# Performance work log

Hardware: AMD Instinct MI355X
Metric: run time of the kernel (lower is better)

The kernel has to match this reference:

```python
import jax, jax.numpy as jnp
import numpy as np

N = 100000      # nodes
E = 1600000     # directed edges (avg degree 16)
DIN, DH, DOUT = 128, 128, 64


def gcn_conv(x, W, b, src, dst, n):
    """PyG GCNConv: out = D^{-1/2} (A + I) D^{-1/2} (x @ W) + b.
    src/dst already include self-loops."""
    deg = jax.ops.segment_sum(jnp.ones_like(src, dtype=x.dtype), dst, num_segments=n)
    dinv = jnp.where(deg > 0, jax.lax.rsqrt(deg), jnp.zeros_like(deg))
    norm = dinv[src] * dinv[dst]                      # [E+N]
    h = x @ W                                         # [N, dout] linear first (PyG)
    msg = h[src] * norm[:, None]                      # gather + scale, [E+N, dout]
    return jax.ops.segment_sum(msg, dst, num_segments=n) + b


def setup_inputs() -> dict:
    key = jax.random.key(0)
    k1, k2, k3 = jax.random.split(key, 3)
    x = jax.random.normal(k1, (N, DIN), dtype=jnp.float32)
    edge_index = jax.random.randint(k2, (2, E), 0, N, dtype=jnp.int64)
    kw1, kw2 = jax.random.split(k3)
    # glorot-style init for the two GCN linear weights
    W1 = jax.random.normal(kw1, (DIN, DH), dtype=jnp.float32) * (1.0 / np.sqrt(DIN))
    b1 = jnp.zeros((DH,), dtype=jnp.float32)
    W2 = jax.random.normal(kw2, (DH, DOUT), dtype=jnp.float32) * (1.0 / np.sqrt(DH))
    b2 = jnp.zeros((DOUT,), dtype=jnp.float32)
    return {"x": x, "W1": W1, "b1": b1, "W2": W2, "b2": b2, "edge_index": edge_index}


def reference(x, W1, b1, W2, b2, edge_index):
    n = x.shape[0]
    loops = jnp.arange(n, dtype=edge_index.dtype)
    src = jnp.concatenate([edge_index[0], loops])     # add self-loops
    dst = jnp.concatenate([edge_index[1], loops])
    h = jax.nn.relu(gcn_conv(x, W1, b1, src, dst, n))
    return gcn_conv(h, W2, b2, src, dst, n)
```

## Files before the change

kernel.cpp:

```cpp
#include <hip/hip_runtime.h>

#define N_NODES 100000
#define N_EDGES 1600000
#define BUCKET_SHIFT 7
#define NB 782
#define BIN_BLOCKS 782
#define GEMM_BLOCKS 1563
#define BCAP 2816
#define AGG1_BLOCKS 3125
#define AGG2_BLOCKS 3125

typedef short bf16x8 __attribute__((ext_vector_type(8)));
typedef float f32x4 __attribute__((ext_vector_type(4)));
typedef float f32x8 __attribute__((ext_vector_type(8)));

__device__ __forceinline__ unsigned short f2bf(float f) {
    unsigned int u = __float_as_uint(f);
    unsigned int r = (u + 0x7FFFu + ((u >> 16) & 1u)) >> 16;
    return (unsigned short)r;
}
__device__ __forceinline__ float bf2f(unsigned short b) {
    return __uint_as_float(((unsigned int)b) << 16);
}
__device__ __forceinline__ void acc8(float* a, uint4 v) {
    a[0] += __uint_as_float(v.x << 16);
    a[1] += __uint_as_float(v.x & 0xFFFF0000u);
    a[2] += __uint_as_float(v.y << 16);
    a[3] += __uint_as_float(v.y & 0xFFFF0000u);
    a[4] += __uint_as_float(v.z << 16);
    a[5] += __uint_as_float(v.z & 0xFFFF0000u);
    a[6] += __uint_as_float(v.w << 16);
    a[7] += __uint_as_float(v.w & 0xFFFF0000u);
}

__global__ __launch_bounds__(256) void k_tw(const float* __restrict__ W1, const float* __restrict__ W2,
                                            unsigned short* __restrict__ w1t, unsigned short* __restrict__ w2t,
                                            int* __restrict__ bcur, int* __restrict__ gcount) {
    int t = blockIdx.x * 256 + threadIdx.x;
    if (t < 16384) {
        int k = t >> 7, c = t & 127;
        w1t[c * 128 + k] = f2bf(W1[t]);
    } else if (t < 24576) {
        int i = t - 16384;
        int k = i >> 6, c = i & 63;
        w2t[c * 128 + k] = f2bf(W2[i]);
    } else if (t - 24576 < NB) {
        bcur[t - 24576] = 0;
    } else if (t - 24576 == NB) {
        *gcount = 0;
    }
}

__global__ __launch_bounds__(256) void k_bin(const int* __restrict__ src, const int* __restrict__ dst,
                                             int* __restrict__ bcur, int* __restrict__ ebuf) {
    __shared__ int hist[NB];
    __shared__ int lbase[NB];
    int t = threadIdx.x;
    int e0 = blockIdx.x * 2048 + t;
    int s[8], d[8];
#pragma unroll
    for (int j = 0; j < 8; ++j) {
        int e = e0 + j * 256;
        bool ok = e < N_EDGES;
        s[j] = ok ? src[e] : -1;
        d[j] = ok ? dst[e] : 0;
    }
    for (int i = t; i < NB; i += 256) hist[i] = 0;
    __syncthreads();
#pragma unroll
    for (int j = 0; j < 8; ++j)
        if (s[j] >= 0) atomicAdd(&hist[d[j] >> BUCKET_SHIFT], 1);
    __syncthreads();
    for (int i = t; i < NB; i += 256)
        if (hist[i] > 0) lbase[i] = atomicAdd(&bcur[i], hist[i]);
    __syncthreads();
    for (int i = t; i < NB; i += 256) hist[i] = 0;
    __syncthreads();
#pragma unroll
    for (int j = 0; j < 8; ++j) {
        if (s[j] >= 0) {
            int b = d[j] >> BUCKET_SHIFT;
            int r = lbase[b] + atomicAdd(&hist[b], 1);
            if (r < BCAP) ebuf[b * BCAP + r] = ((d[j] & 127) << 17) | s[j];
        }
    }
}

__global__ __launch_bounds__(256) void k_bfill3(const int* __restrict__ ebuf, const int* __restrict__ bcur,
                                                int* __restrict__ gcount,
                                                uint2* __restrict__ rowptr2, float* __restrict__ dinv,
                                                int* __restrict__ csr) {
    __shared__ int cnt[128];
    __shared__ int sc[128];
    __shared__ int cur[128];
    __shared__ int s0s;
    int b = blockIdx.x, t = threadIdx.x;
    int node0 = b << BUCKET_SHIFT;
    if (t < 128) cnt[t] = 0;
    int cb = bcur[b];
    int ctot = cb > BCAP ? BCAP : cb;
    if (t == 0) s0s = atomicAdd(gcount, ctot);
    const int* eb = ebuf + b * BCAP;
    __syncthreads();
    for (int i = t; i < ctot; i += 256) atomicAdd(&cnt[eb[i] >> 17], 1);
    __syncthreads();
    int c = (t < 128) ? cnt[t] : 0;
    if (t < 128) sc[t] = c;
    __syncthreads();
    for (int off = 1; off < 128; off <<= 1) {
        int u = (t < 128 && t >= off) ? sc[t - off] : 0;
        __syncthreads();
        if (t < 128) sc[t] += u;
        __syncthreads();
    }
    int s0 = s0s;
    if (t < 128) {
        int p = s0 + sc[t] - c;
        int n = node0 + t;
        if (n < N_NODES) { rowptr2[n] = make_uint2((unsigned)p, (unsigned)c); dinv[n] = rsqrtf(1.0f + (float)c); }
        cur[t] = p;
    }
    __syncthreads();
    for (int i = t; i < ctot; i += 256) {
        int e = eb[i];
        int p = atomicAdd(&cur[e >> 17], 1);
        csr[p] = e & 0x1FFFF;
    }
}

__global__ __launch_bounds__(256) void k_gemm1(const float* __restrict__ x, const unsigned short* __restrict__ w1t,
                                               const float* __restrict__ dinv, unsigned short* __restrict__ hsb) {
    __shared__ unsigned short Xl[64 * 136];
    __shared__ unsigned short Wl[128 * 136];
    int t = threadIdx.x;
    int row0 = blockIdx.x * 64;
    for (int i = t; i < 64 * 32; i += 256) {
        int r = i >> 5, c4 = i & 31;
        int row = row0 + r;
        float4 v = (row < N_NODES) ? ((const float4*)x)[(long long)row * 32 + c4]
                                   : make_float4(0.f, 0.f, 0.f, 0.f);
        ushort4 o;
        o.x = f2bf(v.x); o.y = f2bf(v.y); o.z = f2bf(v.z); o.w = f2bf(v.w);
        *(ushort4*)&Xl[r * 136 + c4 * 4] = o;
    }
    for (int i = t; i < 128 * 16; i += 256) {
        int r = i >> 4, c8 = i & 15;
        *(bf16x8*)&Wl[r * 136 + c8 * 8] = *(const bf16x8*)&w1t[r * 128 + c8 * 8];
    }
    __syncthreads();
    int w = t >> 6, lane = t & 63;
    int nn = lane & 15, quad = lane >> 4;
    bf16x8 a[4];
#pragma unroll
    for (int kt = 0; kt < 4; ++kt)
        a[kt] = *(const bf16x8*)&Xl[(w * 16 + nn) * 136 + kt * 32 + quad * 8];
    f32x4 acc[8];
#pragma unroll
    for (int ct = 0; ct < 8; ++ct) {
        acc[ct] = (f32x4){0.f, 0.f, 0.f, 0.f};
#pragma unroll
        for (int kt = 0; kt < 4; ++kt) {
            bf16x8 b = *(const bf16x8*)&Wl[(ct * 16 + nn) * 136 + kt * 32 + quad * 8];
            acc[ct] = __builtin_amdgcn_mfma_f32_16x16x32_bf16(a[kt], b, acc[ct], 0, 0, 0);
        }
    }
#pragma unroll
    for (int r = 0; r < 4; ++r) {
        int row = row0 + w * 16 + quad * 4 + r;
        float dv = (row < N_NODES) ? dinv[row] : 0.f;
#pragma unroll
        for (int ct = 0; ct < 8; ++ct)
            Xl[(w * 16 + quad * 4 + r) * 136 + ct * 16 + nn] = f2bf(acc[ct][r] * dv);
    }
#pragma unroll
    for (int j = 0; j < 8; ++j) {
        int c = lane + j * 64;
        int r = c >> 5, c4 = c & 31;
        int row = row0 + w * 16 + r;
        if (row < N_NODES)
            ((ushort4*)(hsb + (long long)row * 128))[c4] = *(const ushort4*)&Xl[(w * 16 + r) * 136 + c4 * 4];
    }
}

__global__ __launch_bounds__(256) void k_agg1(const unsigned short* __restrict__ hsb, const uint2* __restrict__ rowptr2,
                                              const int* __restrict__ csr, const float* __restrict__ dinv,
                                              const float* __restrict__ b1, unsigned short* __restrict__ h,
                                              int base) {
    unsigned g = base + ((blockIdx.x * 256 + threadIdx.x) >> 4);
    unsigned li = threadIdx.x & 15;
    if (g >= N_NODES) return;
    unsigned co = li * 8;
    float a[8];
    {
        uint4 sv = *(const uint4*)(hsb + (g << 7) + co);
        a[0] = __uint_as_float(sv.x << 16);
        a[1] = __uint_as_float(sv.x & 0xFFFF0000u);
        a[2] = __uint_as_float(sv.y << 16);
        a[3] = __uint_as_float(sv.y & 0xFFFF0000u);
        a[4] = __uint_as_float(sv.z << 16);
        a[5] = __uint_as_float(sv.z & 0xFFFF0000u);
        a[6] = __uint_as_float(sv.w << 16);
        a[7] = __uint_as_float(sv.w & 0xFFFF0000u);
    }
    uint2 rp = rowptr2[g];
    int k = (int)rp.x, end = (int)(rp.x + rp.y);
    for (; k + 7 < end; k += 8) {
        int i0 = csr[k + 0], i1 = csr[k + 1], i2 = csr[k + 2], i3 = csr[k + 3];
        int i4 = csr[k + 4], i5 = csr[k + 5], i6 = csr[k + 6], i7 = csr[k + 7];
        uint4 v0 = *(const uint4*)(hsb + (((unsigned)i0) << 7) + co);
        uint4 v1 = *(const uint4*)(hsb + (((unsigned)i1) << 7) + co);
        uint4 v2 = *(const uint4*)(hsb + (((unsigned)i2) << 7) + co);
        uint4 v3 = *(const uint4*)(hsb + (((unsigned)i3) << 7) + co);
        uint4 v4 = *(const uint4*)(hsb + (((unsigned)i4) << 7) + co);
        uint4 v5 = *(const uint4*)(hsb + (((unsigned)i5) << 7) + co);
        uint4 v6 = *(const uint4*)(hsb + (((unsigned)i6) << 7) + co);
        uint4 v7 = *(const uint4*)(hsb + (((unsigned)i7) << 7) + co);
        acc8(a, v0); acc8(a, v1); acc8(a, v2); acc8(a, v3);
        acc8(a, v4); acc8(a, v5); acc8(a, v6); acc8(a, v7);
    }
    if (k + 3 < end) {
        int i0 = csr[k + 0], i1 = csr[k + 1], i2 = csr[k + 2], i3 = csr[k + 3];
        uint4 v0 = *(const uint4*)(hsb + (((unsigned)i0) << 7) + co);
        uint4 v1 = *(const uint4*)(hsb + (((unsigned)i1) << 7) + co);
        uint4 v2 = *(const uint4*)(hsb + (((unsigned)i2) << 7) + co);
        uint4 v3 = *(const uint4*)(hsb + (((unsigned)i3) << 7) + co);
        acc8(a, v0); acc8(a, v1); acc8(a, v2); acc8(a, v3);
        k += 4;
    }
    for (; k < end; ++k) {
        uint4 v = *(const uint4*)(hsb + (((unsigned)csr[k]) << 7) + co);
        acc8(a, v);
    }
    float dv = dinv[g];
    f32x8 bb = *(const f32x8*)(b1 + li * 8);
    bf16x8 o;
#pragma unroll
    for (int j = 0; j < 8; ++j)
        o[j] = (short)f2bf(fmaxf(fmaf(dv, a[j], bb[j]), 0.f));
    *(bf16x8*)(h + (g << 7) + co) = o;
}

__global__ __launch_bounds__(256) void k_gemm2(const unsigned short* __restrict__ h, const unsigned short* __restrict__ w2t,
                                               const float* __restrict__ dinv, unsigned short* __restrict__ gsb) {
    __shared__ unsigned short Hl[64 * 136];
    __shared__ unsigned short Wl[64 * 136];
    int t = threadIdx.x;
    int row0 = blockIdx.x * 64;
    for (int i = t; i < 64 * 16; i += 256) {
        int r = i >> 4, c8 = i & 15;
        int row = row0 + r;
        bf16x8 v = (row < N_NODES) ? *(const bf16x8*)&h[(long long)row * 128 + c8 * 8]
                                   : (bf16x8){0, 0, 0, 0, 0, 0, 0, 0};
        *(bf16x8*)&Hl[r * 136 + c8 * 8] = v;
        *(bf16x8*)&Wl[r * 136 + c8 * 8] = *(const bf16x8*)&w2t[r * 128 + c8 * 8];
    }
    __syncthreads();
    int w = t >> 6, lane = t & 63;
    int nn = lane & 15, quad = lane >> 4;
    bf16x8 a[4];
#pragma unroll
    for (int kt = 0; kt < 4; ++kt)
        a[kt] = *(const bf16x8*)&Hl[(w * 16 + nn) * 136 + kt * 32 + quad * 8];
    f32x4 acc[4];
#pragma unroll
    for (int ct = 0; ct < 4; ++ct) {
        acc[ct] = (f32x4){0.f, 0.f, 0.f, 0.f};
#pragma unroll
        for (int kt = 0; kt < 4; ++kt) {
            bf16x8 b = *(const bf16x8*)&Wl[(ct * 16 + nn) * 136 + kt * 32 + quad * 8];
            acc[ct] = __builtin_amdgcn_mfma_f32_16x16x32_bf16(a[kt], b, acc[ct], 0, 0, 0);
        }
    }
#pragma unroll
    for (int r = 0; r < 4; ++r) {
        int row = row0 + w * 16 + quad * 4 + r;
        float dv = (row < N_NODES) ? dinv[row] : 0.f;
#pragma unroll
        for (int ct = 0; ct < 4; ++ct)
            Hl[(w * 16 + quad * 4 + r) * 136 + ct * 16 + nn] = f2bf(acc[ct][r] * dv);
    }
#pragma unroll
    for (int j = 0; j < 4; ++j) {
        int c = lane + j * 64;
        int r = c >> 4, c4 = c & 15;
        int row = row0 + w * 16 + r;
        if (row < N_NODES)
            ((ushort4*)(gsb + (long long)row * 64))[c4] = *(const ushort4*)&Hl[(w * 16 + r) * 136 + c4 * 4];
    }
}

__global__ __launch_bounds__(256) void k_agg2(const unsigned short* __restrict__ gsb, const uint2* __restrict__ rowptr2,
                                              const int* __restrict__ csr, const float* __restrict__ dinv,
                                              const float* __restrict__ b2, float* __restrict__ out) {
    unsigned g = (blockIdx.x * 256 + threadIdx.x) >> 3;
    unsigned li = threadIdx.x & 7;
    if (g >= N_NODES) return;
    unsigned co = li * 8;
    float a[8];
    {
        uint4 sv = *(const uint4*)(gsb + (g << 6) + co);
        a[0] = __uint_as_float(sv.x << 16);
        a[1] = __uint_as_float(sv.x & 0xFFFF0000u);
        a[2] = __uint_as_float(sv.y << 16);
        a[3] = __uint_as_float(sv.y & 0xFFFF0000u);
        a[4] = __uint_as_float(sv.z << 16);
        a[5] = __uint_as_float(sv.z & 0xFFFF0000u);
        a[6] = __uint_as_float(sv.w << 16);
        a[7] = __uint_as_float(sv.w & 0xFFFF0000u);
    }
    uint2 rp = rowptr2[g];
    int k = (int)rp.x, end = (int)(rp.x + rp.y);
    for (; k + 7 < end; k += 8) {
        int i0 = csr[k + 0], i1 = csr[k + 1], i2 = csr[k + 2], i3 = csr[k + 3];
        int i4 = csr[k + 4], i5 = csr[k + 5], i6 = csr[k + 6], i7 = csr[k + 7];
        uint4 v0 = *(const uint4*)(gsb + (((unsigned)i0) << 6) + co);
        uint4 v1 = *(const uint4*)(gsb + (((unsigned)i1) << 6) + co);
        uint4 v2 = *(const uint4*)(gsb + (((unsigned)i2) << 6) + co);
        uint4 v3 = *(const uint4*)(gsb + (((unsigned)i3) << 6) + co);
        uint4 v4 = *(const uint4*)(gsb + (((unsigned)i4) << 6) + co);
        uint4 v5 = *(const uint4*)(gsb + (((unsigned)i5) << 6) + co);
        uint4 v6 = *(const uint4*)(gsb + (((unsigned)i6) << 6) + co);
        uint4 v7 = *(const uint4*)(gsb + (((unsigned)i7) << 6) + co);
        acc8(a, v0); acc8(a, v1); acc8(a, v2); acc8(a, v3);
        acc8(a, v4); acc8(a, v5); acc8(a, v6); acc8(a, v7);
    }
    if (k + 3 < end) {
        int i0 = csr[k + 0], i1 = csr[k + 1], i2 = csr[k + 2], i3 = csr[k + 3];
        uint4 v0 = *(const uint4*)(gsb + (((unsigned)i0) << 6) + co);
        uint4 v1 = *(const uint4*)(gsb + (((unsigned)i1) << 6) + co);
        uint4 v2 = *(const uint4*)(gsb + (((unsigned)i2) << 6) + co);
        uint4 v3 = *(const uint4*)(gsb + (((unsigned)i3) << 6) + co);
        acc8(a, v0); acc8(a, v1); acc8(a, v2); acc8(a, v3);
        k += 4;
    }
    for (; k < end; ++k) {
        uint4 v = *(const uint4*)(gsb + (((unsigned)csr[k]) << 6) + co);
        acc8(a, v);
    }
    float dv = dinv[g];
    f32x8 bb = *(const f32x8*)(b2 + li * 8);
    float4 o0 = make_float4(fmaf(dv, a[0], bb[0]), fmaf(dv, a[1], bb[1]),
                            fmaf(dv, a[2], bb[2]), fmaf(dv, a[3], bb[3]));
    float4 o1 = make_float4(fmaf(dv, a[4], bb[4]), fmaf(dv, a[5], bb[5]),
                            fmaf(dv, a[6], bb[6]), fmaf(dv, a[7], bb[7]));
    float* op = out + ((long long)g << 6) + co;
    *(float4*)op = o0;
    *(float4*)(op + 4) = o1;
}

extern "C" void kernel_launch(void* const* d_in, const int* in_sizes, int n_in,
                              void* d_out, int out_size, void* d_ws, size_t ws_size,
                              hipStream_t stream) {
    const float* x  = (const float*)d_in[0];
    const float* W1 = (const float*)d_in[1];
    const float* b1 = (const float*)d_in[2];
    const float* W2 = (const float*)d_in[3];
    const float* b2 = (const float*)d_in[4];
    const int*   ei = (const int*)d_in[5];
    const int* src = ei;
    const int* dst = ei + N_EDGES;
    float* out = (float*)d_out;

    char* ws = (char*)d_ws;
    int*   csr     = (int*)(ws + 0);
    uint2* rowptr2 = (uint2*)(ws + 6400000);
    float* dinv    = (float*)(ws + 7200000);
    int*   bcur    = (int*)(ws + 7600000);
    int*   gcount  = (int*)(ws + 7603200);
    unsigned short* w1t = (unsigned short*)(ws + 7608448);
    unsigned short* w2t = (unsigned short*)(ws + 7641216);
    int*   ebuf    = (int*)(ws + 8388608);
    unsigned short* hsb = (unsigned short*)(ws + 8388608);
    unsigned short* h   = (unsigned short*)(ws + 59588608);
    unsigned short* gsb = hsb;

    k_tw<<<100, 256, 0, stream>>>(W1, W2, w1t, w2t, bcur, gcount);
    k_bin<<<BIN_BLOCKS, 256, 0, stream>>>(src, dst, bcur, ebuf);
    k_bfill3<<<NB, 256, 0, stream>>>(ebuf, bcur, gcount, rowptr2, dinv, csr);

    k_gemm1<<<GEMM_BLOCKS, 256, 0, stream>>>(x, w1t, dinv, hsb);
    k_agg1<<<AGG1_BLOCKS, 256, 0, stream>>>(hsb, rowptr2, csr, dinv, b1, h, 0);
    k_agg1<<<AGG1_BLOCKS, 256, 0, stream>>>(hsb, rowptr2, csr, dinv, b1, h, 50000);
    k_gemm2<<<GEMM_BLOCKS, 256, 0, stream>>>(h, w2t, dinv, gsb);
    k_agg2<<<AGG2_BLOCKS, 256, 0, stream>>>(gsb, rowptr2, csr, dinv, b2, out);
}
```

Baseline: 286.2 us.

## Replace bucketed CSR build with global-atomic count/scan/fill and merge agg1 launches

```diff
diff --git a/kernel.cpp b/kernel.cpp
--- a/kernel.cpp
+++ b/kernel.cpp
@@ -2,12 +2,10 @@
 
 #define N_NODES 100000
 #define N_EDGES 1600000
-#define BUCKET_SHIFT 7
-#define NB 782
-#define BIN_BLOCKS 782
 #define GEMM_BLOCKS 1563
-#define BCAP 2816
-#define AGG1_BLOCKS 3125
+#define EDGE4_BLOCKS 1563
+#define RP_BLOCKS 782
+#define AGG1_BLOCKS 6250
 #define AGG2_BLOCKS 3125
 
 typedef short bf16x8 __attribute__((ext_vector_type(8)));
@@ -35,7 +33,7 @@
 
 __global__ __launch_bounds__(256) void k_tw(const float* __restrict__ W1, const float* __restrict__ W2,
                                             unsigned short* __restrict__ w1t, unsigned short* __restrict__ w2t,
-                                            int* __restrict__ bcur, int* __restrict__ gcount) {
+                                            int* __restrict__ deg, int* __restrict__ gcount) {
     int t = blockIdx.x * 256 + threadIdx.x;
     if (t < 16384) {
         int k = t >> 7, c = t & 127;
@@ -44,87 +42,69 @@
         int i = t - 16384;
         int k = i >> 6, c = i & 63;
         w2t[c * 128 + k] = f2bf(W2[i]);
-    } else if (t - 24576 < NB) {
-        bcur[t - 24576] = 0;
-    } else if (t - 24576 == NB) {
+    } else if (t - 24576 < N_NODES) {
+        deg[t - 24576] = 0;
+    } else if (t - 24576 == N_NODES) {
         *gcount = 0;
     }
 }
 
-__global__ __launch_bounds__(256) void k_bin(const int* __restrict__ src, const int* __restrict__ dst,
-                                             int* __restrict__ bcur, int* __restrict__ ebuf) {
-    __shared__ int hist[NB];
-    __shared__ int lbase[NB];
-    int t = threadIdx.x;
-    int e0 = blockIdx.x * 2048 + t;
-    int s[8], d[8];
-#pragma unroll
-    for (int j = 0; j < 8; ++j) {
-        int e = e0 + j * 256;
-        bool ok = e < N_EDGES;
-        s[j] = ok ? src[e] : -1;
-        d[j] = ok ? dst[e] : 0;
-    }
-    for (int i = t; i < NB; i += 256) hist[i] = 0;
-    __syncthreads();
-#pragma unroll
-    for (int j = 0; j < 8; ++j)
-        if (s[j] >= 0) atomicAdd(&hist[d[j] >> BUCKET_SHIFT], 1);
-    __syncthreads();
-    for (int i = t; i < NB; i += 256)
-        if (hist[i] > 0) lbase[i] = atomicAdd(&bcur[i], hist[i]);
-    __syncthreads();
-    for (int i = t; i < NB; i += 256) hist[i] = 0;
-    __syncthreads();
-#pragma unroll
-    for (int j = 0; j < 8; ++j) {
-        if (s[j] >= 0) {
-            int b = d[j] >> BUCKET_SHIFT;
-            int r = lbase[b] + atomicAdd(&hist[b], 1);
-            if (r < BCAP) ebuf[b * BCAP + r] = ((d[j] & 127) << 17) | s[j];
-        }
-    }
-}
-
-__global__ __launch_bounds__(256) void k_bfill3(const int* __restrict__ ebuf, const int* __restrict__ bcur,
-                                                int* __restrict__ gcount,
-                                                uint2* __restrict__ rowptr2, float* __restrict__ dinv,
-                                                int* __restrict__ csr) {
-    __shared__ int cnt[128];
+__global__ __launch_bounds__(256) void k_cnt(const int* __restrict__ dst, int* __restrict__ deg) {
+    int i = blockIdx.x * 256 + threadIdx.x;
+    int base = i * 4;
+    if (base + 3 < N_EDGES) {
+        int4 d = *(const int4*)(dst + base);
+        atomicAdd(&deg[d.x], 1);
+        atomicAdd(&deg[d.y], 1);
+        atomicAdd(&deg[d.z], 1);
+        atomicAdd(&deg[d.w], 1);
+    } else {
+        for (int j = base; j < N_EDGES; ++j) atomicAdd(&deg[dst[j]], 1);
+    }
+}
+
+__global__ __launch_bounds__(128) void k_rp(const int* __restrict__ deg, int* __restrict__ gcount,
+                                            uint2* __restrict__ rowptr2, float* __restrict__ dinv,
+                                            int* __restrict__ cur) {
     __shared__ int sc[128];
-    __shared__ int cur[128];
     __shared__ int s0s;
     int b = blockIdx.x, t = threadIdx.x;
-    int node0 = b << BUCKET_SHIFT;
-    if (t < 128) cnt[t] = 0;
-    int cb = bcur[b];
-    int ctot = cb > BCAP ? BCAP : cb;
-    if (t == 0) s0s = atomicAdd(gcount, ctot);
-    const int* eb = ebuf + b * BCAP;
-    __syncthreads();
-    for (int i = t; i < ctot; i += 256) atomicAdd(&cnt[eb[i] >> 17], 1);
-    __syncthreads();
-    int c = (t < 128) ? cnt[t] : 0;
-    if (t < 128) sc[t] = c;
+    int n = b * 128 + t;
+    int c = (n < N_NODES) ? deg[n] : 0;
+    sc[t] = c;
     __syncthreads();
     for (int off = 1; off < 128; off <<= 1) {
-        int u = (t < 128 && t >= off) ? sc[t - off] : 0;
+        int u = (t >= off) ? sc[t - off] : 0;
         __syncthreads();
-        if (t < 128) sc[t] += u;
+        sc[t] += u;
         __syncthreads();
     }
-    int s0 = s0s;
-    if (t < 128) {
-        int p = s0 + sc[t] - c;
-        int n = node0 + t;
-        if (n < N_NODES) { rowptr2[n] = make_uint2((unsigned)p, (unsigned)c); dinv[n] = rsqrtf(1.0f + (float)c); }
-        cur[t] = p;
-    }
+    if (t == 127) s0s = atomicAdd(gcount, sc[127]);
     __syncthreads();
-    for (int i = t; i < ctot; i += 256) {
-        int e = eb[i];
-        int p = atomicAdd(&cur[e >> 17], 1);
-        csr[p] = e & 0x1FFFF;
+    int p = s0s + sc[t] - c;
+    if (n < N_NODES) {
+        rowptr2[n] = make_uint2((unsigned)p, (unsigned)c);
+        dinv[n] = rsqrtf(1.0f + (float)c);
+        cur[n] = p;
+    }
+}
+
+__global__ __launch_bounds__(256) void k_fill(const int* __restrict__ src, const int* __restrict__ dst,
+                                              int* __restrict__ cur, int* __restrict__ csr) {
+    int i = blockIdx.x * 256 + threadIdx.x;
+    int base = i * 4;
+    if (base + 3 < N_EDGES) {
+        int4 s = *(const int4*)(src + base);
+        int4 d = *(const int4*)(dst + base);
+        int p0 = atomicAdd(&cur[d.x], 1); csr[p0] = s.x;
+        int p1 = atomicAdd(&cur[d.y], 1); csr[p1] = s.y;
+        int p2 = atomicAdd(&cur[d.z], 1); csr[p2] = s.z;
+        int p3 = atomicAdd(&cur[d.w], 1); csr[p3] = s.w;
+    } else {
+        for (int j = base; j < N_EDGES; ++j) {
+            int p = atomicAdd(&cur[dst[j]], 1);
+            csr[p] = src[j];
+        }
     }
 }
 
@@ -184,9 +164,8 @@
 
 __global__ __launch_bounds__(256) void k_agg1(const unsigned short* __restrict__ hsb, const uint2* __restrict__ rowptr2,
                                               const int* __restrict__ csr, const float* __restrict__ dinv,
-                                              const float* __restrict__ b1, unsigned short* __restrict__ h,
-                                              int base) {
-    unsigned g = base + ((blockIdx.x * 256 + threadIdx.x) >> 4);
+                                              const float* __restrict__ b1, unsigned short* __restrict__ h) {
+    unsigned g = (blockIdx.x * 256 + threadIdx.x) >> 4;
     unsigned li = threadIdx.x & 15;
     if (g >= N_NODES) return;
     unsigned co = li * 8;
@@ -365,22 +344,22 @@
     int*   csr     = (int*)(ws + 0);
     uint2* rowptr2 = (uint2*)(ws + 6400000);
     float* dinv    = (float*)(ws + 7200000);
-    int*   bcur    = (int*)(ws + 7600000);
-    int*   gcount  = (int*)(ws + 7603200);
-    unsigned short* w1t = (unsigned short*)(ws + 7608448);
-    unsigned short* w2t = (unsigned short*)(ws + 7641216);
-    int*   ebuf    = (int*)(ws + 8388608);
-    unsigned short* hsb = (unsigned short*)(ws + 8388608);
+    int*   deg     = (int*)(ws + 7600000);
+    int*   cur     = (int*)(ws + 8000000);
+    int*   gcount  = (int*)(ws + 8400000);
+    unsigned short* w1t = (unsigned short*)(ws + 8400128);
+    unsigned short* w2t = (unsigned short*)(ws + 8432896);
+    unsigned short* hsb = (unsigned short*)(ws + 8650752);
     unsigned short* h   = (unsigned short*)(ws + 59588608);
     unsigned short* gsb = hsb;
 
-    k_tw<<<100, 256, 0, stream>>>(W1, W2, w1t, w2t, bcur, gcount);
-    k_bin<<<BIN_BLOCKS, 256, 0, stream>>>(src, dst, bcur, ebuf);
-    k_bfill3<<<NB, 256, 0, stream>>>(ebuf, bcur, gcount, rowptr2, dinv, csr);
+    k_tw<<<487, 256, 0, stream>>>(W1, W2, w1t, w2t, deg, gcount);
+    k_cnt<<<EDGE4_BLOCKS, 256, 0, stream>>>(dst, deg);
+    k_rp<<<RP_BLOCKS, 128, 0, stream>>>(deg, gcount, rowptr2, dinv, cur);
+    k_fill<<<EDGE4_BLOCKS, 256, 0, stream>>>(src, dst, cur, csr);
 
     k_gemm1<<<GEMM_BLOCKS, 256, 0, stream>>>(x, w1t, dinv, hsb);
-    k_agg1<<<AGG1_BLOCKS, 256, 0, stream>>>(hsb, rowptr2, csr, dinv, b1, h, 0);
-    k_agg1<<<AGG1_BLOCKS, 256, 0, stream>>>(hsb, rowptr2, csr, dinv, b1, h, 50000);
+    k_agg1<<<AGG1_BLOCKS, 256, 0, stream>>>(hsb, rowptr2, csr, dinv, b1, h);
     k_gemm2<<<GEMM_BLOCKS, 256, 0, stream>>>(h, w2t, dinv, gsb);
     k_agg2<<<AGG2_BLOCKS, 256, 0, stream>>>(gsb, rowptr2, csr, dinv, b2, out);
 }
```

New measurement: 417.3 us. 45.8% more time.
